# Kernel tuning notes

Hardware: AMD Instinct MI355X
Metric: run time of the kernel (lower is better)

The kernel has to match this reference:

```python
import jax, jax.numpy as jnp
import numpy as np

B, S, D, H = 2, 2048, 1024, 16
HD = D // H
SCALING = HD ** -0.5


def _length_mask(lengths, seqlen):
    return (jnp.arange(seqlen)[None, :] < jnp.asarray(lengths)[:, None]).astype(jnp.int32)


def setup_inputs() -> dict:
    key = jax.random.key(0)
    ks = jax.random.split(key, 10)
    std = D ** -0.5
    inp = {
        "hidden_states": jax.random.normal(ks[0], (B, S, D), dtype=jnp.float32),
        "Wq": jax.random.normal(ks[1], (D, D), dtype=jnp.float32) * std,
        "bq": jax.random.normal(ks[2], (D,), dtype=jnp.float32) * 0.02,
        "Wk": jax.random.normal(ks[3], (D, D), dtype=jnp.float32) * std,
        "bk": jax.random.normal(ks[4], (D,), dtype=jnp.float32) * 0.02,
        "Wv": jax.random.normal(ks[5], (D, D), dtype=jnp.float32) * std,
        "bv": jax.random.normal(ks[6], (D,), dtype=jnp.float32) * 0.02,
        "Wo": jax.random.normal(ks[7], (D, D), dtype=jnp.float32) * std,
        "bo": jax.random.normal(ks[8], (D,), dtype=jnp.float32) * 0.02,
        # variable valid lengths per batch element (padding at the end)
        "query_mask_1d": _length_mask([S, S - 512], S),
        "key_mask_1d": _length_mask([S, S - 512], S),
    }
    return inp


def reference(hidden_states, Wq, bq, Wk, bk, Wv, bv, Wo, bo, query_mask_1d, key_mask_1d):
    bsz, tgt_len, _ = hidden_states.shape
    # projections (dropout p=0 / eval -> identity)
    q = (hidden_states @ Wq + bq) * SCALING
    k = hidden_states @ Wk + bk
    v = hidden_states @ Wv + bv
    q = q.reshape(bsz, tgt_len, H, HD).transpose(0, 2, 1, 3)  # [B,H,S,HD]
    k = k.reshape(bsz, -1, H, HD).transpose(0, 2, 1, 3)
    v = v.reshape(bsz, -1, H, HD).transpose(0, 2, 1, 3)

    scores = jnp.einsum("bhqd,bhkd->bhqk", q, k)  # [B,H,S,S]
    q_valid = (query_mask_1d != 0)[:, None, :, None]  # [B,1,S,1]
    k_valid = (key_mask_1d != 0)[:, None, None, :]    # [B,1,1,S]
    # masked_fill(-inf) on padded keys; padded-query rows would be all -inf ->
    # softmax NaN -> nan_to_num(0). We compute the same result NaN-free by
    # zeroing the scores of padded-query rows and zeroing their probs after.
    s = jnp.where(k_valid, scores, -jnp.inf)
    s = jnp.where(q_valid, s, 0.0)
    attn_weights = jax.nn.softmax(s, axis=-1) * q_valid  # == softmax + nan_to_num

    attn_output = jnp.einsum("bhqk,bhkd->bhqd", attn_weights, v)
    attn_output = attn_output.transpose(0, 2, 1, 3).reshape(bsz, tgt_len, D)
    attn_output = attn_output @ Wo + bo
    return attn_output
```

## Files before the change

kernel.cpp:

```cpp
#include <hip/hip_runtime.h>
#include <stdint.h>

#define BB 2
#define SS 2048
#define DD 1024
#define HH 16
#define HDIM 64
#define MTOT (BB*SS)
#define QK_SCALE_LOG2E 0.180336880f

typedef unsigned short u16;
typedef __attribute__((ext_vector_type(8))) __bf16 bf16x8;
typedef __attribute__((ext_vector_type(4))) float f32x4;

static __device__ __forceinline__ float exp2_hw(float x) {
    return __builtin_amdgcn_exp2f(x);
}

static __device__ __forceinline__ u16 f2bu(float f) {
    union { float f; uint32_t u; } c; c.f = f;
    uint32_t u = c.u + 0x7fffu + ((c.u >> 16) & 1u);
    return (u16)(u >> 16);
}

static __device__ __forceinline__ u16 f2b_hw(float f) {
    __bf16 b = (__bf16)f;
    union { __bf16 b; u16 u; } c; c.b = b;
    return c.u;
}

static __device__ __forceinline__ uint32_t cvt_pk_bf16(float lo, float hi) {
    uint32_t r;
    asm("v_cvt_pk_bf16_f32 %0, %1, %2" : "=v"(r) : "v"(lo), "v"(hi));
    return r;
}

static __device__ __forceinline__ void gload_lds16(const void* g, void* l) {
    __builtin_amdgcn_global_load_lds(
        (const __attribute__((address_space(1))) uint32_t*)(g),
        (__attribute__((address_space(3))) uint32_t*)(l),
        16, 0, 0);
}

__global__ void k_convert_x(const float* __restrict__ x, u16* __restrict__ xb) {
    int i = (blockIdx.x * blockDim.x + threadIdx.x) * 4;
    float4 v = *(const float4*)(x + i);
    ushort4 o;
    o.x = f2bu(v.x); o.y = f2bu(v.y); o.z = f2bu(v.z); o.w = f2bu(v.w);
    *(ushort4*)(xb + i) = o;
}

__global__ void k_transpose_w(const float* __restrict__ Wq, const float* __restrict__ Wk,
                              const float* __restrict__ Wv, const float* __restrict__ Wo,
                              u16* __restrict__ Wqkv_t, u16* __restrict__ Wo_t) {
    __shared__ float tile[32][33];
    const int which = blockIdx.z;
    const float* W = (which == 0) ? Wq : (which == 1) ? Wk : (which == 2) ? Wv : Wo;
    u16* dst = (which < 3) ? (Wqkv_t + (size_t)which * DD * DD) : Wo_t;
    const int n0 = blockIdx.x * 32, k0 = blockIdx.y * 32;
    const int tx = threadIdx.x, ty = threadIdx.y;
    #pragma unroll
    for (int i = 0; i < 32; i += 8)
        tile[ty + i][tx] = W[(size_t)(k0 + ty + i) * DD + (n0 + tx)];
    __syncthreads();
    #pragma unroll
    for (int i = 0; i < 32; i += 8)
        dst[(size_t)(n0 + ty + i) * DD + (k0 + tx)] = f2bu(tile[tx][ty + i]);
}

__global__ __launch_bounds__(256) void k_gemm_qkv(
    const u16* __restrict__ Xb, const u16* __restrict__ Wt,
    const float* __restrict__ bq, const float* __restrict__ bk_, const float* __restrict__ bv,
    u16* __restrict__ Qb, u16* __restrict__ Kb, u16* __restrict__ Vt)
{
    __shared__ u16 As[2][128 * 64];
    __shared__ u16 Bs[2][128 * 64];
    const int m0 = blockIdx.y * 128, n0 = blockIdx.x * 128;
    const int t = threadIdx.x;
    const int lane = t & 63, w = t >> 6;
    const int wm = (w >> 1) << 6, wn = (w & 1) << 6;
    const int lr = lane & 15, lg = lane >> 4;

    f32x4 acc[4][4] = {};

    auto stage = [&](int buf, int k0) {
        #pragma unroll
        for (int i = 0; i < 4; ++i) {
            int off = (t + (i << 8)) << 4;
            int row = off >> 7, colb = off & 127;
            int scol = colb ^ ((row & 7) << 4);
            gload_lds16(Xb + (size_t)(m0 + row) * DD + k0 + (scol >> 1), (char*)As[buf] + off);
            gload_lds16(Wt + (size_t)(n0 + row) * DD + k0 + (scol >> 1), (char*)Bs[buf] + off);
        }
    };

    stage(0, 0);
    __syncthreads();

    int cur = 0;
    for (int kt = 0; kt < 16; ++kt) {
        if (kt < 15) stage(cur ^ 1, (kt + 1) << 6);
        #pragma unroll
        for (int ks = 0; ks < 2; ++ks) {
            bf16x8 a[4], b[4];
            #pragma unroll
            for (int i = 0; i < 4; ++i) {
                const int row = wm + (i << 4) + lr;
                a[i] = *(const bf16x8*)((const char*)As[cur] + row * 128 + (((ks << 6) + (lg << 4)) ^ ((row & 7) << 4)));
            }
            #pragma unroll
            for (int i = 0; i < 4; ++i) {
                const int row = wn + (i << 4) + lr;
                b[i] = *(const bf16x8*)((const char*)Bs[cur] + row * 128 + (((ks << 6) + (lg << 4)) ^ ((row & 7) << 4)));
            }
            #pragma unroll
            for (int mi = 0; mi < 4; ++mi)
                #pragma unroll
                for (int ni = 0; ni < 4; ++ni)
                    acc[mi][ni] = __builtin_amdgcn_mfma_f32_16x16x32_bf16(a[mi], b[ni], acc[mi][ni], 0, 0, 0);
        }
        __syncthreads();
        cur ^= 1;
    }

    #pragma unroll
    for (int mi = 0; mi < 4; ++mi) {
        #pragma unroll
        for (int ni = 0; ni < 4; ++ni) {
            const int n = n0 + wn + (ni << 4) + lr;
            const int mbase = m0 + wm + (mi << 4) + (lg << 2);
            const int b_ = mbase >> 11;
            const int s_ = mbase & 2047;
            if (n < DD) {
                const float bias = bq[n];
                const int hh = n >> 6, d = n & 63;
                u16* dstp = Qb + (((size_t)b_ * HH + hh) * SS + s_) * HDIM + d;
                #pragma unroll
                for (int r = 0; r < 4; ++r)
                    dstp[(size_t)r * HDIM] = f2bu((acc[mi][ni][r] + bias) * QK_SCALE_LOG2E);
            } else if (n < 2 * DD) {
                const int nn = n - DD;
                const float bias = bk_[nn];
                const int hh = nn >> 6, d = nn & 63;
                u16* dstp = Kb + (((size_t)b_ * HH + hh) * SS + s_) * HDIM + d;
                #pragma unroll
                for (int r = 0; r < 4; ++r)
                    dstp[(size_t)r * HDIM] = f2bu(acc[mi][ni][r] + bias);
            } else {
                const int nn = n - 2 * DD;
                const float bias = bv[nn];
                const int hh = nn >> 6, d = nn & 63;
                ushort4 pk;
                pk.x = f2bu(acc[mi][ni][0] + bias);
                pk.y = f2bu(acc[mi][ni][1] + bias);
                pk.z = f2bu(acc[mi][ni][2] + bias);
                pk.w = f2bu(acc[mi][ni][3] + bias);
                *(ushort4*)(Vt + (((size_t)b_ * HH + hh) * HDIM + d) * SS + s_) = pk;
            }
        }
    }
}

__global__ __launch_bounds__(256) void k_attn(
    const u16* __restrict__ Qb, const u16* __restrict__ Kb, const u16* __restrict__ Vt,
    const int* __restrict__ qmask, const int* __restrict__ kmask,
    u16* __restrict__ X2)
{
    const int blk = blockIdx.x;
    const int qt = blk & 31;
    const int h = (blk >> 5) & 15;
    const int b_ = blk >> 9;
    const int t = threadIdx.x;
    const int lane = t & 63, w = t >> 6;
    const int lr = lane & 15, lg = lane >> 4;

    __shared__ u16 Ks[2][64 * 64];
    __shared__ u16 Vs[2][64 * 64];
    __shared__ u16 Ps[4][16 * 64];

    const int q0 = qt << 6;
    const size_t bh = (size_t)b_ * HH + h;
    const u16* Qbase = Qb + bh * SS * HDIM;
    const char* KbaseB = (const char*)(Kb + bh * SS * HDIM);
    const char* VbaseB = (const char*)(Vt + bh * HDIM * SS);

    if (qmask[b_ * SS + q0] == 0) {
        #pragma unroll
        for (int r = 0; r < 4; ++r) {
            const int q = q0 + (w << 4) + (lg << 2) + r;
            #pragma unroll
            for (int nf = 0; nf < 4; ++nf)
                X2[((size_t)b_ * SS + q) * DD + (h << 6) + (nf << 4) + lr] = 0;
        }
        return;
    }

    int kv = (lane < 32) ? kmask[b_ * SS + (lane << 6)] : 0;
    unsigned long long bal = __ballot(kv != 0);
    const int nkt = __popcll(bal);

    bf16x8 qf[2];
    #pragma unroll
    for (int ks = 0; ks < 2; ++ks)
        qf[ks] = *(const bf16x8*)(Qbase + (size_t)(q0 + (w << 4) + lr) * HDIM + (ks << 5) + (lg << 3));

    bf16x8 vones;
    #pragma unroll
    for (int i = 0; i < 8; ++i) vones[i] = (__bf16)1.0f;

    f32x4 o[4] = {};
    f32x4 lacc = {};

    auto stage = [&](int buf, int kb) {
        #pragma unroll
        for (int i = 0; i < 2; ++i) {
            int off = (t + (i << 8)) << 4;
            int row = off >> 7, colb = off & 127;
            int scol = colb ^ ((row & 7) << 4);
            gload_lds16(KbaseB + (size_t)(kb + row) * 128 + scol, (char*)Ks[buf] + off);
            gload_lds16(VbaseB + ((size_t)row * SS + (size_t)kb) * 2 + scol, (char*)Vs[buf] + off);
        }
    };

    if (nkt > 0) stage(0, 0);
    __syncthreads();

    u16* P = Ps[w];

    int cur = 0;
    for (int kt = 0; kt < nkt; ++kt) {
        const int kb = kt << 6;
        if (kt + 1 < nkt) stage(cur ^ 1, kb + 64);

        f32x4 sf[4] = {};
        #pragma unroll
        for (int ks = 0; ks < 2; ++ks) {
            #pragma unroll
            for (int f = 0; f < 4; ++f) {
                const int krow = (f << 4) + lr;
                const int kcol = ((ks << 6) + (lg << 4)) ^ ((krow & 7) << 4);
                bf16x8 kf = *(const bf16x8*)((const char*)Ks[cur] + krow * 128 + kcol);
                sf[f] = __builtin_amdgcn_mfma_f32_16x16x32_bf16(kf, qf[ks], sf[f], 0, 0, 0);
            }
        }
        if (kt == nkt - 1) {
            #pragma unroll
            for (int f = 0; f < 4; ++f) {
                #pragma unroll
                for (int r = 0; r < 4; ++r) {
                    if (kmask[b_ * SS + kb + (f << 4) + (lg << 2) + r] == 0)
                        sf[f][r] = -1e30f;
                }
            }
        }
        #pragma unroll
        for (int f = 0; f < 4; ++f)
            #pragma unroll
            for (int r = 0; r < 4; ++r)
                sf[f][r] = exp2_hw(sf[f][r]);

        #pragma unroll
        for (int f = 0; f < 4; ++f) {
            uint2 pk;
            pk.x = cvt_pk_bf16(sf[f][0], sf[f][1]);
            pk.y = cvt_pk_bf16(sf[f][2], sf[f][3]);
            *(uint2*)((char*)P + (((lr << 7) + (f << 5) + (lg << 3)) ^ ((lr & 7) << 4))) = pk;
        }

        #pragma unroll
        for (int ks = 0; ks < 2; ++ks) {
            bf16x8 pa = *(const bf16x8*)((const char*)P + (((lr << 7) + (ks << 6) + (lg << 4)) ^ ((lr & 7) << 4)));
            lacc = __builtin_amdgcn_mfma_f32_16x16x32_bf16(pa, vones, lacc, 0, 0, 0);
            #pragma unroll
            for (int nf = 0; nf < 4; ++nf) {
                const int vrow = (nf << 4) + lr;
                const int vcol = ((ks << 6) + (lg << 4)) ^ ((vrow & 7) << 4);
                bf16x8 vb = *(const bf16x8*)((const char*)Vs[cur] + vrow * 128 + vcol);
                o[nf] = __builtin_amdgcn_mfma_f32_16x16x32_bf16(pa, vb, o[nf], 0, 0, 0);
            }
        }
        __syncthreads();
        cur ^= 1;
    }

    #pragma unroll
    for (int r = 0; r < 4; ++r) {
        const int q = q0 + (w << 4) + (lg << 2) + r;
        float l = lacc[r];
        float inv = (l > 0.f) ? __builtin_amdgcn_rcpf(l) : 0.f;
        if (qmask[b_ * SS + q] == 0) inv = 0.f;
        #pragma unroll
        for (int nf = 0; nf < 4; ++nf)
            X2[((size_t)b_ * SS + q) * DD + (h << 6) + (nf << 4) + lr] = f2b_hw(o[nf][r] * inv);
    }
}

__global__ __launch_bounds__(256) void k_gemm_out(
    const u16* __restrict__ X2, const u16* __restrict__ Wot,
    const float* __restrict__ bo, float* __restrict__ out)
{
    __shared__ u16 As[2][128 * 64];
    __shared__ u16 Bs[2][128 * 64];
    const int m0 = blockIdx.y * 128, n0 = blockIdx.x * 128;
    const int t = threadIdx.x;
    const int lane = t & 63, w = t >> 6;
    const int wm = (w >> 1) << 6, wn = (w & 1) << 6;
    const int lr = lane & 15, lg = lane >> 4;

    f32x4 acc[4][4] = {};

    auto stage = [&](int buf, int k0) {
        #pragma unroll
        for (int i = 0; i < 4; ++i) {
            int off = (t + (i << 8)) << 4;
            int row = off >> 7, colb = off & 127;
            int scol = colb ^ ((row & 7) << 4);
            gload_lds16(X2 + (size_t)(m0 + row) * DD + k0 + (scol >> 1), (char*)As[buf] + off);
            gload_lds16(Wot + (size_t)(n0 + row) * DD + k0 + (scol >> 1), (char*)Bs[buf] + off);
        }
    };

    stage(0, 0);
    __syncthreads();

    int cur = 0;
    for (int kt = 0; kt < 16; ++kt) {
        if (kt < 15) stage(cur ^ 1, (kt + 1) << 6);
        #pragma unroll
        for (int ks = 0; ks < 2; ++ks) {
            bf16x8 a[4], b[4];
            #pragma unroll
            for (int i = 0; i < 4; ++i) {
                const int row = wm + (i << 4) + lr;
                a[i] = *(const bf16x8*)((const char*)As[cur] + row * 128 + (((ks << 6) + (lg << 4)) ^ ((row & 7) << 4)));
            }
            #pragma unroll
            for (int i = 0; i < 4; ++i) {
                const int row = wn + (i << 4) + lr;
                b[i] = *(const bf16x8*)((const char*)Bs[cur] + row * 128 + (((ks << 6) + (lg << 4)) ^ ((row & 7) << 4)));
            }
            #pragma unroll
            for (int mi = 0; mi < 4; ++mi)
                #pragma unroll
                for (int ni = 0; ni < 4; ++ni)
                    acc[mi][ni] = __builtin_amdgcn_mfma_f32_16x16x32_bf16(a[mi], b[ni], acc[mi][ni], 0, 0, 0);
        }
        __syncthreads();
        cur ^= 1;
    }

    #pragma unroll
    for (int mi = 0; mi < 4; ++mi) {
        #pragma unroll
        for (int ni = 0; ni < 4; ++ni) {
            const int n = n0 + wn + (ni << 4) + lr;
            const int mbase = m0 + wm + (mi << 4) + (lg << 2);
            const float bias = bo[n];
            #pragma unroll
            for (int r = 0; r < 4; ++r)
                out[(size_t)(mbase + r) * DD + n] = acc[mi][ni][r] + bias;
        }
    }
}

extern "C" void kernel_launch(void* const* d_in, const int* in_sizes, int n_in,
                              void* d_out, int out_size, void* d_ws, size_t ws_size,
                              hipStream_t stream) {
    const float* hs = (const float*)d_in[0];
    const float* Wq = (const float*)d_in[1];
    const float* bq = (const float*)d_in[2];
    const float* Wk = (const float*)d_in[3];
    const float* bk = (const float*)d_in[4];
    const float* Wv = (const float*)d_in[5];
    const float* bv = (const float*)d_in[6];
    const float* Wo = (const float*)d_in[7];
    const float* bo = (const float*)d_in[8];
    const int* qm = (const int*)d_in[9];
    const int* km = (const int*)d_in[10];
    float* out = (float*)d_out;

    char* ws = (char*)d_ws;
    const size_t MB = 1024 * 1024;
    u16* Xb  = (u16*)(ws + 0);
    u16* Wt3 = (u16*)(ws + 8 * MB);
    u16* Wot = (u16*)(ws + 14 * MB);
    u16* Qb  = (u16*)(ws + 16 * MB);
    u16* Kb  = (u16*)(ws + 24 * MB);
    u16* Vt  = (u16*)(ws + 32 * MB);
    u16* X2  = (u16*)(ws + 40 * MB);

    k_convert_x<<<dim3(MTOT * DD / 1024), dim3(256), 0, stream>>>(hs, Xb);
    k_transpose_w<<<dim3(32, 32, 4), dim3(32, 8), 0, stream>>>(Wq, Wk, Wv, Wo, Wt3, Wot);
    k_gemm_qkv<<<dim3(24, 32), dim3(256), 0, stream>>>(Xb, Wt3, bq, bk, bv, Qb, Kb, Vt);
    k_attn<<<dim3(1024), dim3(256), 0, stream>>>(Qb, Kb, Vt, qm, km, X2);
    k_gemm_out<<<dim3(8, 32), dim3(256), 0, stream>>>(X2, Wot, bo, out);
}
```

Before: 130.6 us.

## Rewrite QKV GEMM with 256x256 tiles, 8 waves, and phased load pipeline

The QKV projection GEMM moves from 128x128 tiles with 4 waves to 256x256 tiles with 8 waves per block. The K loop becomes an explicitly phased schedule that interleaves half-tile global-to-LDS loads with MFMA groups, using manual barriers, waitcnts, sched_barrier and s_setprio. A block-index swizzle is added for L2 locality, and the epilogue picks Q/K/V per block. The goal is higher arithmetic intensity and better overlap of memory with MFMA. The cost is 128KB of LDS per block and only 192 blocks, which may underfill the GPU's compute units.

```diff
diff --git a/kernel.cpp b/kernel.cpp
--- a/kernel.cpp
+++ b/kernel.cpp
@@ -68,93 +68,146 @@
         dst[(size_t)(n0 + ty + i) * DD + (k0 + tx)] = f2bu(tile[tx][ty + i]);
 }
 
-__global__ __launch_bounds__(256) void k_gemm_qkv(
+#define PH_BODY(BUF, Q, READB, STAGECODE, TAILWAIT)                           \
+  { bf16x8 afr[2][2];                                                         \
+    _Pragma("unroll") for (int m2 = 0; m2 < 2; ++m2)                          \
+      _Pragma("unroll") for (int ks = 0; ks < 2; ++ks)                        \
+        afr[m2][ks] = rdA(BUF, 2*(Q)+m2, ks);                                 \
+    if (READB) {                                                              \
+      _Pragma("unroll") for (int nf = 0; nf < 4; ++nf)                        \
+        _Pragma("unroll") for (int ks = 0; ks < 2; ++ks)                      \
+          bfr[nf][ks] = rdB(BUF, nf, ks);                                     \
+    }                                                                         \
+    STAGECODE;                                                                \
+    __builtin_amdgcn_s_barrier();                                             \
+    asm volatile("s_waitcnt lgkmcnt(0)" ::: "memory");                        \
+    __builtin_amdgcn_sched_barrier(0);                                        \
+    __builtin_amdgcn_s_setprio(1);                                            \
+    _Pragma("unroll") for (int m2 = 0; m2 < 2; ++m2)                          \
+      _Pragma("unroll") for (int nf = 0; nf < 4; ++nf)                        \
+        _Pragma("unroll") for (int ks = 0; ks < 2; ++ks)                      \
+          acc[2*(Q)+m2][nf] = __builtin_amdgcn_mfma_f32_16x16x32_bf16(        \
+              afr[m2][ks], bfr[nf][ks], acc[2*(Q)+m2][nf], 0, 0, 0);          \
+    __builtin_amdgcn_s_setprio(0);                                            \
+    TAILWAIT;                                                                 \
+    __builtin_amdgcn_s_barrier();                                             \
+  }
+
+__global__ __launch_bounds__(512, 2) void k_gemm_qkv(
     const u16* __restrict__ Xb, const u16* __restrict__ Wt,
     const float* __restrict__ bq, const float* __restrict__ bk_, const float* __restrict__ bv,
     u16* __restrict__ Qb, u16* __restrict__ Kb, u16* __restrict__ Vt)
 {
-    __shared__ u16 As[2][128 * 64];
-    __shared__ u16 Bs[2][128 * 64];
-    const int m0 = blockIdx.y * 128, n0 = blockIdx.x * 128;
+    __shared__ u16 As[2][256 * 64];
+    __shared__ u16 Bs[2][256 * 64];
+
+    const int flat = blockIdx.y * 12 + blockIdx.x;
+    const int swz = (flat & 7) * 24 + (flat >> 3);
+    const int bx = swz % 12, by = swz / 12;
+    const int m0 = by << 8, n0 = bx << 8;
+
     const int t = threadIdx.x;
     const int lane = t & 63, w = t >> 6;
-    const int wm = (w >> 1) << 6, wn = (w & 1) << 6;
+    const int wm = (w >> 2) << 7, wn = (w & 3) << 6;
     const int lr = lane & 15, lg = lane >> 4;
 
-    f32x4 acc[4][4] = {};
-
-    auto stage = [&](int buf, int k0) {
-        #pragma unroll
-        for (int i = 0; i < 4; ++i) {
-            int off = (t + (i << 8)) << 4;
+    const u16* Asrc = Xb + (size_t)m0 * DD;
+    const u16* Bsrc = Wt + (size_t)n0 * DD;
+
+    f32x4 acc[8][4] = {};
+    bf16x8 bfr[4][2];
+
+    auto stgA = [&](int buf, int half, int tt) {
+        #pragma unroll
+        for (int r = 0; r < 2; ++r) {
+            int off = (t + (r << 9)) << 4;
             int row = off >> 7, colb = off & 127;
             int scol = colb ^ ((row & 7) << 4);
-            gload_lds16(Xb + (size_t)(m0 + row) * DD + k0 + (scol >> 1), (char*)As[buf] + off);
-            gload_lds16(Wt + (size_t)(n0 + row) * DD + k0 + (scol >> 1), (char*)Bs[buf] + off);
-        }
-    };
-
-    stage(0, 0);
-    __syncthreads();
-
-    int cur = 0;
-    for (int kt = 0; kt < 16; ++kt) {
-        if (kt < 15) stage(cur ^ 1, (kt + 1) << 6);
-        #pragma unroll
-        for (int ks = 0; ks < 2; ++ks) {
-            bf16x8 a[4], b[4];
-            #pragma unroll
-            for (int i = 0; i < 4; ++i) {
-                const int row = wm + (i << 4) + lr;
-                a[i] = *(const bf16x8*)((const char*)As[cur] + row * 128 + (((ks << 6) + (lg << 4)) ^ ((row & 7) << 4)));
-            }
-            #pragma unroll
-            for (int i = 0; i < 4; ++i) {
-                const int row = wn + (i << 4) + lr;
-                b[i] = *(const bf16x8*)((const char*)Bs[cur] + row * 128 + (((ks << 6) + (lg << 4)) ^ ((row & 7) << 4)));
-            }
-            #pragma unroll
-            for (int mi = 0; mi < 4; ++mi)
-                #pragma unroll
-                for (int ni = 0; ni < 4; ++ni)
-                    acc[mi][ni] = __builtin_amdgcn_mfma_f32_16x16x32_bf16(a[mi], b[ni], acc[mi][ni], 0, 0, 0);
-        }
-        __syncthreads();
-        cur ^= 1;
-    }
-
-    #pragma unroll
-    for (int mi = 0; mi < 4; ++mi) {
-        #pragma unroll
-        for (int ni = 0; ni < 4; ++ni) {
-            const int n = n0 + wn + (ni << 4) + lr;
-            const int mbase = m0 + wm + (mi << 4) + (lg << 2);
+            gload_lds16(Asrc + (size_t)((half << 7) + row) * DD + (tt << 6) + (scol >> 1),
+                        (char*)As[buf] + (half << 14) + off);
+        }
+    };
+    auto stgB = [&](int buf, int half, int tt) {
+        #pragma unroll
+        for (int r = 0; r < 2; ++r) {
+            int off = (t + (r << 9)) << 4;
+            int row = off >> 7, colb = off & 127;
+            int scol = colb ^ ((row & 7) << 4);
+            gload_lds16(Bsrc + (size_t)((half << 7) + row) * DD + (tt << 6) + (scol >> 1),
+                        (char*)Bs[buf] + (half << 14) + off);
+        }
+    };
+
+    auto rdA = [&](int buf, int mf, int ks) {
+        const int row = wm + (mf << 4) + lr;
+        const int col = ((ks << 6) + (lg << 4)) ^ ((row & 7) << 4);
+        return *(const bf16x8*)((const char*)As[buf] + row * 128 + col);
+    };
+    auto rdB = [&](int buf, int nf, int ks) {
+        const int row = wn + (nf << 4) + lr;
+        const int col = ((ks << 6) + (lg << 4)) ^ ((row & 7) << 4);
+        return *(const bf16x8*)((const char*)Bs[buf] + row * 128 + col);
+    };
+
+    stgA(0, 0, 0); stgA(0, 1, 0); stgB(0, 0, 0); stgB(0, 1, 0);
+    stgB(1, 0, 1); stgB(1, 1, 1);
+    asm volatile("s_waitcnt vmcnt(4)" ::: "memory");
+    __builtin_amdgcn_s_barrier();
+
+    #pragma unroll 1
+    for (int i = 0; i < 7; ++i) {
+        const int t1 = 2 * i + 1, t2 = 2 * i + 2, t3 = 2 * i + 3;
+        PH_BODY(0, 0, true,  { stgA(1, 0, t1); }, {});
+        PH_BODY(0, 1, false, { stgA(1, 1, t1); }, {});
+        PH_BODY(0, 2, false, { stgB(0, 0, t2); }, {});
+        PH_BODY(0, 3, false, { stgB(0, 1, t2); },
+                { asm volatile("s_waitcnt vmcnt(4)" ::: "memory"); });
+        PH_BODY(1, 0, true,  { stgA(0, 0, t2); }, {});
+        PH_BODY(1, 1, false, { stgA(0, 1, t2); }, {});
+        PH_BODY(1, 2, false, { stgB(1, 0, t3); }, {});
+        PH_BODY(1, 3, false, { stgB(1, 1, t3); },
+                { asm volatile("s_waitcnt vmcnt(4)" ::: "memory"); });
+    }
+    PH_BODY(0, 0, true,  { stgA(1, 0, 15); }, {});
+    PH_BODY(0, 1, false, { stgA(1, 1, 15); }, {});
+    PH_BODY(0, 2, false, {}, {});
+    PH_BODY(0, 3, false, {},
+            { asm volatile("s_waitcnt vmcnt(0)" ::: "memory"); });
+    PH_BODY(1, 0, true,  {}, {});
+    PH_BODY(1, 1, false, {}, {});
+    PH_BODY(1, 2, false, {}, {});
+    PH_BODY(1, 3, false, {}, {});
+
+    const int which = n0 >> 10;
+    #pragma unroll
+    for (int mf = 0; mf < 8; ++mf) {
+        #pragma unroll
+        for (int nf = 0; nf < 4; ++nf) {
+            const int n = n0 + wn + (nf << 4) + lr;
+            const int mbase = m0 + wm + (mf << 4) + (lg << 2);
             const int b_ = mbase >> 11;
             const int s_ = mbase & 2047;
-            if (n < DD) {
-                const float bias = bq[n];
-                const int hh = n >> 6, d = n & 63;
+            const int nn = n & 1023;
+            const int hh = nn >> 6, d = nn & 63;
+            if (which == 0) {
+                const float bias = bq[nn];
                 u16* dstp = Qb + (((size_t)b_ * HH + hh) * SS + s_) * HDIM + d;
                 #pragma unroll
                 for (int r = 0; r < 4; ++r)
-                    dstp[(size_t)r * HDIM] = f2bu((acc[mi][ni][r] + bias) * QK_SCALE_LOG2E);
-            } else if (n < 2 * DD) {
-                const int nn = n - DD;
+                    dstp[(size_t)r * HDIM] = f2bu((acc[mf][nf][r] + bias) * QK_SCALE_LOG2E);
+            } else if (which == 1) {
                 const float bias = bk_[nn];
-                const int hh = nn >> 6, d = nn & 63;
                 u16* dstp = Kb + (((size_t)b_ * HH + hh) * SS + s_) * HDIM + d;
                 #pragma unroll
                 for (int r = 0; r < 4; ++r)
-                    dstp[(size_t)r * HDIM] = f2bu(acc[mi][ni][r] + bias);
+                    dstp[(size_t)r * HDIM] = f2bu(acc[mf][nf][r] + bias);
             } else {
-                const int nn = n - 2 * DD;
                 const float bias = bv[nn];
-                const int hh = nn >> 6, d = nn & 63;
                 ushort4 pk;
-                pk.x = f2bu(acc[mi][ni][0] + bias);
-                pk.y = f2bu(acc[mi][ni][1] + bias);
-                pk.z = f2bu(acc[mi][ni][2] + bias);
-                pk.w = f2bu(acc[mi][ni][3] + bias);
+                pk.x = f2bu(acc[mf][nf][0] + bias);
+                pk.y = f2bu(acc[mf][nf][1] + bias);
+                pk.z = f2bu(acc[mf][nf][2] + bias);
+                pk.w = f2bu(acc[mf][nf][3] + bias);
                 *(ushort4*)(Vt + (((size_t)b_ * HH + hh) * HDIM + d) * SS + s_) = pk;
             }
         }
@@ -299,8 +352,8 @@
     const u16* __restrict__ X2, const u16* __restrict__ Wot,
     const float* __restrict__ bo, float* __restrict__ out)
 {
-    __shared__ u16 As[2][128 * 64];
-    __shared__ u16 Bs[2][128 * 64];
+    __shared__ u16 As2[2][128 * 64];
+    __shared__ u16 Bs2[2][128 * 64];
     const int m0 = blockIdx.y * 128, n0 = blockIdx.x * 128;
     const int t = threadIdx.x;
     const int lane = t & 63, w = t >> 6;
@@ -315,8 +368,8 @@
             int off = (t + (i << 8)) << 4;
             int row = off >> 7, colb = off & 127;
             int scol = colb ^ ((row & 7) << 4);
-            gload_lds16(X2 + (size_t)(m0 + row) * DD + k0 + (scol >> 1), (char*)As[buf] + off);
-            gload_lds16(Wot + (size_t)(n0 + row) * DD + k0 + (scol >> 1), (char*)Bs[buf] + off);
+            gload_lds16(X2 + (size_t)(m0 + row) * DD + k0 + (scol >> 1), (char*)As2[buf] + off);
+            gload_lds16(Wot + (size_t)(n0 + row) * DD + k0 + (scol >> 1), (char*)Bs2[buf] + off);
         }
     };
 
@@ -332,12 +385,12 @@
             #pragma unroll
             for (int i = 0; i < 4; ++i) {
                 const int row = wm + (i << 4) + lr;
-                a[i] = *(const bf16x8*)((const char*)As[cur] + row * 128 + (((ks << 6) + (lg << 4)) ^ ((row & 7) << 4)));
+                a[i] = *(const bf16x8*)((const char*)As2[cur] + row * 128 + (((ks << 6) + (lg << 4)) ^ ((row & 7) << 4)));
             }
             #pragma unroll
             for (int i = 0; i < 4; ++i) {
                 const int row = wn + (i << 4) + lr;
-                b[i] = *(const bf16x8*)((const char*)Bs[cur] + row * 128 + (((ks << 6) + (lg << 4)) ^ ((row & 7) << 4)));
+                b[i] = *(const bf16x8*)((const char*)Bs2[cur] + row * 128 + (((ks << 6) + (lg << 4)) ^ ((row & 7) << 4)));
             }
             #pragma unroll
             for (int mi = 0; mi < 4; ++mi)
@@ -391,7 +444,7 @@
 
     k_convert_x<<<dim3(MTOT * DD / 1024), dim3(256), 0, stream>>>(hs, Xb);
     k_transpose_w<<<dim3(32, 32, 4), dim3(32, 8), 0, stream>>>(Wq, Wk, Wv, Wo, Wt3, Wot);
-    k_gemm_qkv<<<dim3(24, 32), dim3(256), 0, stream>>>(Xb, Wt3, bq, bk, bv, Qb, Kb, Vt);
+    k_gemm_qkv<<<dim3(12, 16), dim3(512), 0, stream>>>(Xb, Wt3, bq, bk, bv, Qb, Kb, Vt);
     k_attn<<<dim3(1024), dim3(256), 0, stream>>>(Qb, Kb, Vt, qm, km, X2);
     k_gemm_out<<<dim3(8, 32), dim3(256), 0, stream>>>(X2, Wot, bo, out);
 }
```

Result: faster. 123.1 us (-5.7%).
